# Performance work log

Hardware: AMD Instinct MI355X
Metric: run time of the kernel (lower is better)

## Reference

```python
import jax, jax.numpy as jnp
import numpy as np

NUM_TOKENS = 8192
HIDDEN = 4096
NUM_EXPERTS = 64
TOP_K = 8


def setup_inputs() -> dict:
    key = jax.random.key(0)
    k1, k2, k3 = jax.random.split(key, 3)
    tokens = jax.random.normal(k1, (NUM_TOKENS, HIDDEN), dtype=jnp.float32)
    token_probs = jax.random.uniform(k2, (NUM_TOKENS, NUM_EXPERTS), dtype=jnp.float32)
    # exactly TOP_K experts per token -> static num_out_tokens
    scores = jax.random.normal(k3, (NUM_TOKENS, NUM_EXPERTS))
    _, topk_idx = jax.lax.top_k(scores, TOP_K)  # [T, K]
    rows = jnp.arange(NUM_TOKENS)[:, None]
    routing_map = jnp.zeros((NUM_TOKENS, NUM_EXPERTS), dtype=bool).at[rows, topk_idx].set(True)
    return {
        "tokens": tokens,
        "token_probs": token_probs,
        "routing_map": routing_map,
        "num_out_tokens": NUM_TOKENS * TOP_K,
    }


def reference(tokens, token_probs, routing_map, num_out_tokens):
    # Fallback (non-fused) path of TurboTokenPermuter.forward.
    num_tokens, _ = tokens.shape
    # routing_map.bool().T -> [E, T]; masked_select in row-major order =
    # for each expert (in order), the token ids routed to it (in token order).
    flat_mask = routing_map.T.reshape(-1)  # [E*T]
    # stable argsort of ~mask puts flat positions of True entries first, in order
    perm = jnp.argsort(~flat_mask, stable=True)[:num_out_tokens]  # flat E*T indices
    sorted_indices = (perm % num_tokens).astype(jnp.int32)  # token ids (column index)
    permuted_probs = token_probs.T.reshape(-1)[perm]
    permuted_input = tokens[sorted_indices]  # index_select along dim 0
    return permuted_input, permuted_probs, sorted_indices
```

## Files before the change

kernel.cpp:

```cpp
#include <hip/hip_runtime.h>
#include <stdint.h>

#define NTOK   8192
#define NEXP   64
#define HID    4096
#define TOPK   8
#define OUTROW 65536
#define CHUNK  256
#define NCHUNK 32
#define NPART  2048

typedef float f32x4 __attribute__((ext_vector_type(4)));
typedef unsigned long long u64;

__global__ void mask_rank_kernel(const int* __restrict__ map,
                                 u64* __restrict__ masks,
                                 u64* __restrict__ tok_rank,
                                 int* __restrict__ pcnt) {
    int c = blockIdx.x;
    int tid = threadIdx.x;
    int w = tid >> 6, lane = tid & 63;

    __shared__ u64 sm[CHUNK];
    __shared__ unsigned short rnk[CHUNK][NEXP];
    __shared__ int wtot[4][NEXP];

    int t0 = c * CHUNK + w * 64;
#pragma unroll 8
    for (int i = 0; i < 64; ++i) {
        int v = map[(size_t)(t0 + i) * NEXP + lane];
        u64 bal = __ballot(v != 0);
        if (lane == 0) sm[w * 64 + i] = bal;
    }
    __syncthreads();

    int cnt = 0;
#pragma unroll 8
    for (int i = 0; i < 64; ++i) {
        u64 mk = sm[w * 64 + i];
        rnk[w * 64 + i][lane] = (unsigned short)cnt;
        cnt += (int)((mk >> lane) & 1ull);
    }
    wtot[w][lane] = cnt;
    __syncthreads();

    u64 mk = sm[tid];
    masks[c * CHUNK + tid] = mk;
    int myw = tid >> 6;
    u64 tmp = mk;
    u64 packed = 0;
#pragma unroll
    for (int j = 0; j < TOPK; ++j) {
        int e = tmp ? (__ffsll((long long)tmp) - 1) : 0;
        tmp &= tmp - 1;
        int r = rnk[tid][e];
        if (myw > 0) r += wtot[0][e];
        if (myw > 1) r += wtot[1][e];
        if (myw > 2) r += wtot[2][e];
        packed |= (u64)(r & 0xff) << (8 * j);
    }
    tok_rank[c * CHUNK + tid] = packed;

    if (tid < NEXP)
        pcnt[tid * NCHUNK + c] = wtot[0][tid] + wtot[1][tid] + wtot[2][tid] + wtot[3][tid];
}

__global__ void scan_kernel(const int* __restrict__ pcnt, int* __restrict__ poffs) {
    __shared__ int s[256];
    int tid = threadIdx.x;
    int v[8];
    int sum = 0;
#pragma unroll
    for (int i = 0; i < 8; ++i) { v[i] = pcnt[tid * 8 + i]; sum += v[i]; }
    s[tid] = sum;
    __syncthreads();
    for (int off = 1; off < 256; off <<= 1) {
        int x = (tid >= off) ? s[tid - off] : 0;
        __syncthreads();
        s[tid] += x;
        __syncthreads();
    }
    int base = (tid == 0) ? 0 : s[tid - 1];
#pragma unroll
    for (int i = 0; i < 8; ++i) { poffs[tid * 8 + i] = base; base += v[i]; }
}

__global__ void mega_kernel(const u64* __restrict__ masks,
                            const u64* __restrict__ tok_rank,
                            const float* __restrict__ probs,
                            const int* __restrict__ poffs,
                            const float* __restrict__ tokens,
                            float* __restrict__ out_rows,
                            float* __restrict__ out_probs,
                            float* __restrict__ out_idx) {
    int b = blockIdx.x;
    int t = b >> 1, h = b & 1;
    int c = t >> 8;
    int tid = threadIdx.x;

    const f32x4* sp = (const f32x4*)(tokens + (size_t)t * HID) + h * 512;
    f32x4 v0 = __builtin_nontemporal_load(sp + tid);
    f32x4 v1 = __builtin_nontemporal_load(sp + tid + 256);

    u64 mk = tok_rank ? masks[t] : 0;
    mk = masks[t];
    u64 rk = tok_rank[t];

    f32x4* dp[TOPK];
    u64 tmp = mk;
#pragma unroll
    for (int j = 0; j < TOPK; ++j) {
        int e = tmp ? (__ffsll((long long)tmp) - 1) : 0;
        tmp &= tmp - 1;
        int pos = poffs[e * NCHUNK + c] + (int)((rk >> (8 * j)) & 0xff);
        if ((unsigned)pos >= OUTROW) pos = 0;
        dp[j] = (f32x4*)(out_rows + (size_t)pos * HID) + h * 512;
        if (h == 0 && tid == j) {
            out_idx[pos] = (float)t;
            out_probs[pos] = probs[(size_t)t * NEXP + e];
        }
    }

#pragma unroll
    for (int j = 0; j < TOPK; ++j) {
        __builtin_nontemporal_store(v0, dp[j] + tid);
        __builtin_nontemporal_store(v1, dp[j] + tid + 256);
    }
}

extern "C" void kernel_launch(void* const* d_in, const int* in_sizes, int n_in,
                              void* d_out, int out_size, void* d_ws, size_t ws_size,
                              hipStream_t stream) {
    const float* tokens = (const float*)d_in[0];
    const float* probs  = (const float*)d_in[1];
    const int*   map    = (const int*)d_in[2];

    float* out_rows  = (float*)d_out;
    float* out_probs = out_rows + (size_t)OUTROW * HID;
    float* out_idx   = out_probs + OUTROW;

    u64* masks    = (u64*)d_ws;
    u64* tok_rank = masks + NTOK;
    int* pcnt     = (int*)(tok_rank + NTOK);
    int* poffs    = pcnt + NPART;

    mask_rank_kernel<<<NCHUNK, CHUNK, 0, stream>>>(map, masks, tok_rank, pcnt);
    scan_kernel<<<1, CHUNK, 0, stream>>>(pcnt, poffs);
    mega_kernel<<<NTOK * 2, CHUNK, 0, stream>>>(masks, tok_rank, probs, poffs, tokens,
                                                out_rows, out_probs, out_idx);
}
```

Baseline: 267.3 us.

## Switch scatter to destination-ordered gather with per-chunk sorted entry lists

The mask kernel now builds a per-chunk list of (token, expert, rank) entries sorted by expert, instead of per-token packed ranks. The copy kernel is reorganized so each block handles 32 output rows that are contiguous within an expert segment. It gathers full source rows and writes destination rows in mostly sequential order, and block ids are mapped so each XCD handles whole chunks. This trades one read per token fanned out to eight writes for eight reads per token, each landing on a sequential write stream, and it relies on L2 reuse of the source rows within a chunk.

```diff
diff --git a/kernel.cpp b/kernel.cpp
--- a/kernel.cpp
+++ b/kernel.cpp
@@ -9,13 +9,16 @@
 #define CHUNK  256
 #define NCHUNK 32
 #define NPART  2048
+#define LISTSZ (CHUNK * TOPK)
+#define RPB    32
 
 typedef float f32x4 __attribute__((ext_vector_type(4)));
 typedef unsigned long long u64;
 
-__global__ void mask_rank_kernel(const int* __restrict__ map,
-                                 u64* __restrict__ masks,
-                                 u64* __restrict__ tok_rank,
+#define PACK(t, e, r) (((unsigned)(t) << 14) | ((unsigned)(e) << 8) | (unsigned)(r))
+
+__global__ void mask_list_kernel(const int* __restrict__ map,
+                                 unsigned* __restrict__ chunk_list,
                                  int* __restrict__ pcnt) {
     int c = blockIdx.x;
     int tid = threadIdx.x;
@@ -24,6 +27,8 @@
     __shared__ u64 sm[CHUNK];
     __shared__ unsigned short rnk[CHUNK][NEXP];
     __shared__ int wtot[4][NEXP];
+    __shared__ int pref[NEXP];
+    __shared__ unsigned s_list[LISTSZ];
 
     int t0 = c * CHUNK + w * 64;
 #pragma unroll 8
@@ -44,23 +49,34 @@
     wtot[w][lane] = cnt;
     __syncthreads();
 
+    if (tid == 0) {
+        int acc = 0;
+        for (int e = 0; e < NEXP; ++e) {
+            pref[e] = acc;
+            acc += wtot[0][e] + wtot[1][e] + wtot[2][e] + wtot[3][e];
+        }
+    }
+    __syncthreads();
+
     u64 mk = sm[tid];
-    masks[c * CHUNK + tid] = mk;
-    int myw = tid >> 6;
+    int t = c * CHUNK + tid;
     u64 tmp = mk;
-    u64 packed = 0;
 #pragma unroll
     for (int j = 0; j < TOPK; ++j) {
         int e = tmp ? (__ffsll((long long)tmp) - 1) : 0;
         tmp &= tmp - 1;
         int r = rnk[tid][e];
-        if (myw > 0) r += wtot[0][e];
-        if (myw > 1) r += wtot[1][e];
-        if (myw > 2) r += wtot[2][e];
-        packed |= (u64)(r & 0xff) << (8 * j);
+        if (w > 0) r += wtot[0][e];
+        if (w > 1) r += wtot[1][e];
+        if (w > 2) r += wtot[2][e];
+        int flatk = pref[e] + r;
+        s_list[flatk & (LISTSZ - 1)] = PACK(t, e, r);
     }
-    tok_rank[c * CHUNK + tid] = packed;
+    __syncthreads();
 
+#pragma unroll
+    for (int i = 0; i < TOPK; ++i)
+        chunk_list[c * LISTSZ + i * CHUNK + tid] = s_list[i * CHUNK + tid];
     if (tid < NEXP)
         pcnt[tid * NCHUNK + c] = wtot[0][tid] + wtot[1][tid] + wtot[2][tid] + wtot[3][tid];
 }
@@ -85,46 +101,53 @@
     for (int i = 0; i < 8; ++i) { poffs[tid * 8 + i] = base; base += v[i]; }
 }
 
-__global__ void mega_kernel(const u64* __restrict__ masks,
-                            const u64* __restrict__ tok_rank,
-                            const float* __restrict__ probs,
-                            const int* __restrict__ poffs,
-                            const float* __restrict__ tokens,
-                            float* __restrict__ out_rows,
-                            float* __restrict__ out_probs,
-                            float* __restrict__ out_idx) {
-    int b = blockIdx.x;
-    int t = b >> 1, h = b & 1;
-    int c = t >> 8;
+__global__ void seg_kernel(const unsigned* __restrict__ chunk_list,
+                           const float* __restrict__ probs,
+                           const int* __restrict__ poffs,
+                           const float* __restrict__ tokens,
+                           float* __restrict__ out_rows,
+                           float* __restrict__ out_probs,
+                           float* __restrict__ out_idx) {
+    int bid = blockIdx.x;
+    int xcd = bid & 7;
+    int i4  = bid >> 3;
+    int c = xcd + 8 * (i4 >> 6);
+    int j = i4 & 63;
     int tid = threadIdx.x;
 
-    const f32x4* sp = (const f32x4*)(tokens + (size_t)t * HID) + h * 512;
-    f32x4 v0 = __builtin_nontemporal_load(sp + tid);
-    f32x4 v1 = __builtin_nontemporal_load(sp + tid + 256);
+    __shared__ int s_src[RPB];
+    __shared__ int s_dst[RPB];
 
-    u64 mk = tok_rank ? masks[t] : 0;
-    mk = masks[t];
-    u64 rk = tok_rank[t];
+    if (tid < RPB) {
+        unsigned ent = chunk_list[c * LISTSZ + j * RPB + tid];
+        int t = ent >> 14;
+        int e = (ent >> 8) & 63;
+        int r = ent & 255;
+        int pos = poffs[e * NCHUNK + c] + r;
+        if ((unsigned)pos >= OUTROW) pos = 0;
+        s_src[tid] = t;
+        s_dst[tid] = pos;
+        out_idx[pos] = (float)t;
+        out_probs[pos] = probs[(size_t)t * NEXP + e];
+    }
+    __syncthreads();
 
-    f32x4* dp[TOPK];
-    u64 tmp = mk;
-#pragma unroll
-    for (int j = 0; j < TOPK; ++j) {
-        int e = tmp ? (__ffsll((long long)tmp) - 1) : 0;
-        tmp &= tmp - 1;
-        int pos = poffs[e * NCHUNK + c] + (int)((rk >> (8 * j)) & 0xff);
-        if ((unsigned)pos >= OUTROW) pos = 0;
-        dp[j] = (f32x4*)(out_rows + (size_t)pos * HID) + h * 512;
-        if (h == 0 && tid == j) {
-            out_idx[pos] = (float)t;
-            out_probs[pos] = probs[(size_t)t * NEXP + e];
-        }
-    }
-
-#pragma unroll
-    for (int j = 0; j < TOPK; ++j) {
-        __builtin_nontemporal_store(v0, dp[j] + tid);
-        __builtin_nontemporal_store(v1, dp[j] + tid + 256);
+    for (int i = 0; i < RPB; i += 2) {
+        int s0 = s_src[i], s1 = s_src[i + 1];
+        const f32x4* sp0 = (const f32x4*)(tokens + (size_t)s0 * HID);
+        const f32x4* sp1 = (const f32x4*)(tokens + (size_t)s1 * HID);
+        f32x4* dp0 = (f32x4*)(out_rows + (size_t)s_dst[i] * HID);
+        f32x4* dp1 = (f32x4*)(out_rows + (size_t)s_dst[i + 1] * HID);
+        f32x4 a0 = sp0[tid], a1 = sp0[tid + 256], a2 = sp0[tid + 512], a3 = sp0[tid + 768];
+        f32x4 b0 = sp1[tid], b1 = sp1[tid + 256], b2 = sp1[tid + 512], b3 = sp1[tid + 768];
+        __builtin_nontemporal_store(a0, dp0 + tid);
+        __builtin_nontemporal_store(a1, dp0 + tid + 256);
+        __builtin_nontemporal_store(a2, dp0 + tid + 512);
+        __builtin_nontemporal_store(a3, dp0 + tid + 768);
+        __builtin_nontemporal_store(b0, dp1 + tid);
+        __builtin_nontemporal_store(b1, dp1 + tid + 256);
+        __builtin_nontemporal_store(b2, dp1 + tid + 512);
+        __builtin_nontemporal_store(b3, dp1 + tid + 768);
     }
 }
 
@@ -139,13 +162,12 @@
     float* out_probs = out_rows + (size_t)OUTROW * HID;
     float* out_idx   = out_probs + OUTROW;
 
-    u64* masks    = (u64*)d_ws;
-    u64* tok_rank = masks + NTOK;
-    int* pcnt     = (int*)(tok_rank + NTOK);
-    int* poffs    = pcnt + NPART;
+    unsigned* chunk_list = (unsigned*)d_ws;
+    int* pcnt  = (int*)(chunk_list + NTOK * TOPK);
+    int* poffs = pcnt + NPART;
 
-    mask_rank_kernel<<<NCHUNK, CHUNK, 0, stream>>>(map, masks, tok_rank, pcnt);
+    mask_list_kernel<<<NCHUNK, CHUNK, 0, stream>>>(map, chunk_list, pcnt);
     scan_kernel<<<1, CHUNK, 0, stream>>>(pcnt, poffs);
-    mega_kernel<<<NTOK * 2, CHUNK, 0, stream>>>(masks, tok_rank, probs, poffs, tokens,
-                                                out_rows, out_probs, out_idx);
+    seg_kernel<<<NPART, CHUNK, 0, stream>>>(chunk_list, probs, poffs, tokens,
+                                            out_rows, out_probs, out_idx);
 }
```

New measurement: 240.5 us. 10.0% less time.
